# Optimization experiments

Measured on AMD Instinct MI355X. Metric: run time of the kernel, lower is better.

Reference implementation:

```python
import jax, jax.numpy as jnp
import numpy as np

N_NODES = 50000
N_EDGES = 800000
MUL = 16            # multiplicity of each irrep (16x0e + 16x1o)
RADIAL_IN = 8       # radial basis size
RADIAL_HID = 64
N_PATHS = 5         # TP paths: s*Y0->s, v.Yv->s, s*Yv->v, v*Y0->v, v x Yv->v
NUM_SPECIES = 4
AVG_NEIGH = 16.0


def setup_inputs() -> dict:
    key = jax.random.key(0)
    ks = jax.random.split(key, 16)
    inp = {
        'node_scalars': jax.random.normal(ks[0], (N_NODES, MUL), jnp.float32),
        'node_vectors': jax.random.normal(ks[1], (N_NODES, MUL * 3), jnp.float32),
        'edge_sh': jax.random.normal(ks[2], (N_EDGES, 4), jnp.float32),
        'radial_emb': jax.random.uniform(ks[3], (N_EDGES, RADIAL_IN), jnp.float32),
        'senders': jax.random.randint(ks[4], (N_EDGES,), 0, N_NODES, jnp.int32),
        'receivers': jax.random.randint(ks[5], (N_EDGES,), 0, N_NODES, jnp.int32),
        'species': jax.random.randint(ks[6], (N_NODES,), 0, NUM_SPECIES, jnp.int32),
        # learned params (fan-in scaled)
        'W_in_s': jax.random.normal(ks[7], (MUL, MUL), jnp.float32) / np.sqrt(MUL),
        'W_in_v': jax.random.normal(ks[8], (MUL, MUL), jnp.float32) / np.sqrt(MUL),
        'mlp_w1': jax.random.normal(ks[9], (RADIAL_IN, RADIAL_HID), jnp.float32) / np.sqrt(RADIAL_IN),
        'mlp_b1': jnp.zeros((RADIAL_HID,), jnp.float32),
        'mlp_w2': jax.random.normal(ks[10], (RADIAL_HID, N_PATHS * MUL), jnp.float32) / np.sqrt(RADIAL_HID),
        'W_out_s': jax.random.normal(ks[11], (2 * MUL, 2 * MUL), jnp.float32) / np.sqrt(2 * MUL),
        'W_out_v': jax.random.normal(ks[12], (3 * MUL, MUL), jnp.float32) / np.sqrt(3 * MUL),
        'sc_s': jax.random.normal(ks[13], (NUM_SPECIES, MUL, 2 * MUL), jnp.float32) / np.sqrt(MUL),
        'sc_v': jax.random.normal(ks[14], (NUM_SPECIES, MUL, MUL), jnp.float32) / np.sqrt(MUL),
    }
    return inp


def reference(node_scalars, node_vectors, edge_sh, radial_emb, senders, receivers,
              species, W_in_s, W_in_v, mlp_w1, mlp_b1, mlp_w2, W_out_s, W_out_v,
              sc_s, sc_v):
    N = node_scalars.shape[0]
    inv_sqrt_deg = 1.0 / np.sqrt(AVG_NEIGH)

    # ---- input per-irrep linear ----
    s = node_scalars @ W_in_s                                  # [N,16]
    v_in = node_vectors.reshape(N, MUL, 3)
    v = jnp.einsum('nuc,uw->nwc', v_in, W_in_v)                # [N,16,3]

    # ---- gather sender features ----
    xs = s[senders]                                            # [E,16]
    xv = v[senders]                                            # [E,16,3]
    Y0 = edge_sh[:, :1]                                        # [E,1] l=0 SH
    Yv = edge_sh[:, 1:4]                                       # [E,3] l=1 SH

    # ---- radial MLP -> per-path tensor-product weights ----
    h = jax.nn.silu(radial_emb @ mlp_w1 + mlp_b1)              # [E,64]
    w = (h @ mlp_w2).reshape(-1, N_PATHS, MUL)                 # [E,5,16]

    # ---- CG tensor product (uvu) messages ----
    m_s1 = w[:, 0] * xs * Y0                                   # 0e x 0e -> 0e
    m_s2 = w[:, 1] * jnp.einsum('euc,ec->eu', xv, Yv)          # 1o x 1o -> 0e (dot)
    m_v1 = w[:, 2, :, None] * xs[:, :, None] * Yv[:, None, :]  # 0e x 1o -> 1o
    m_v2 = w[:, 3, :, None] * xv * Y0[:, :, None]              # 1o x 0e -> 1o
    m_v3 = w[:, 4, :, None] * jnp.cross(xv, Yv[:, None, :])    # 1o x 1o -> 1o (cross)

    # ---- scatter-sum to receivers + neighbour normalization ----
    m_s = jnp.concatenate([m_s1, m_s2], axis=-1)               # [E,32]
    m_v = jnp.concatenate([m_v1, m_v2, m_v3], axis=1)          # [E,48,3]
    a_s = jax.ops.segment_sum(m_s, receivers, num_segments=N) * inv_sqrt_deg
    a_v = jax.ops.segment_sum(m_v, receivers, num_segments=N) * inv_sqrt_deg

    # ---- output per-irrep linear ----
    pre_s = a_s @ W_out_s                                      # [N,32]
    pre_v = jnp.einsum('nuc,uw->nwc', a_v, W_out_v)            # [N,16,3]

    # ---- species-dependent self connection ----
    pre_s = pre_s + jnp.einsum('nu,nuw->nw', node_scalars, sc_s[species])
    pre_v = pre_v + jnp.einsum('nuc,nuw->nwc', v_in, sc_v[species])

    # ---- gate nonlinearity ----
    out_s = jax.nn.silu(pre_s[:, :MUL])                        # scalar outputs
    gates = jax.nn.sigmoid(pre_s[:, MUL:])                     # gate scalars
    out_v = pre_v * gates[:, :, None]

    # ---- resnet ----
    out_s = out_s + node_scalars
    out_v = out_v + v_in

    return jnp.concatenate([out_s, out_v.reshape(N, MUL * 3)], axis=-1)
```

## Files before the change

kernel.cpp:

```cpp
#include <hip/hip_runtime.h>
#include <hip/hip_bf16.h>

typedef unsigned short u16;
typedef unsigned int   u32;
typedef _Float16 h2 __attribute__((ext_vector_type(2)));
typedef short s8v __attribute__((ext_vector_type(8)));
typedef float f4v __attribute__((ext_vector_type(4)));
typedef u16 u16x4 __attribute__((ext_vector_type(4)));

#define N_NODES 50000
#define N_EDGES 800000
#define NCH   2
#define RPC   25000
#define CHMAX 409600

#define RPB   250
#define NBINS 200
#define EPB   4096
#define NBB   ((N_EDGES+EPB-1)/EPB)

#define WB_W1H  0
#define WB_B1   256
#define WB_W2F  320
#define WB_WINS 2880
#define WB_WINV 3136
#define WB_WOS  3392
#define WB_WOV  4416
#define WB_SCS  5184
#define WB_SCV  7232
#define WB_FLAG 8256
#define OFF_SV16 8260
#define IDX_BCNT 1608260
#define IDX_BOF2 1608516
#define IDX_BCUR 1608772
#define IDX_OFFS 1658260
#define IDX_BUCK 1758262
#define IDX_EEID 2558264
#define OFF_ER16 3358264
#define OFF_WPA  3758264
#define OFF_WPB  16865464
#define OFF_YB   20142264
#define OFF_SND  21780664
#define ACC_OFF  21985464

__device__ __forceinline__ float bf2f(u16 v){
  union { u32 u; float f; } x; x.u = ((u32)v) << 16; return x.f;
}
__device__ __forceinline__ u16 f2bf(float f){
  u32 u = __float_as_uint(f);
  u32 lsb = (u >> 16) & 1u;
  u32 r = u + 0x7fffu + lsb;
  return (u16)(r >> 16);
}
__device__ __forceinline__ float ldx(const void* p, long long i, int isf){
  return isf ? ((const float*)p)[i] : bf2f(((const u16*)p)[i]);
}
__device__ __forceinline__ u32 pkh2(float a, float b){
  union { u32 u; h2 v; } x; x.v.x = (_Float16)a; x.v.y = (_Float16)b; return x.u;
}
__device__ __forceinline__ float dot2(h2 a, u32 w, float c){
  union { u32 u; h2 v; } x; x.u = w;
#if __has_builtin(__builtin_amdgcn_fdot2)
  return __builtin_amdgcn_fdot2(a, x.v, c, false);
#else
  return c + (float)a.x*(float)x.v.x + (float)a.y*(float)x.v.y;
#endif
}
__device__ __forceinline__ float sigmoidf_(float x){ return 1.f/(1.f + __expf(-x)); }

__global__ void detect_dtype(const u32* __restrict__ remb_raw, int* __restrict__ flag){
  int t = threadIdx.x;
  u32 w = remb_raw[t];
  u32 lo = w & 0xffffu, hi = w >> 16;
  int okl = ((lo & 0x8000u) == 0) && (((lo >> 7) & 0xffu) <= 126u);
  int okh = ((hi & 0x8000u) == 0) && (((hi >> 7) & 0xffu) <= 126u);
  unsigned long long bad = __ballot(!(okl && okh));
  if (t == 0) *flag = (bad != 0ull) ? 1 : 0;
}

__global__ void prep_weights(const void* __restrict__ w1, const void* __restrict__ b1g,
                             const void* __restrict__ w2, const void* __restrict__ wins,
                             const void* __restrict__ winv, const void* __restrict__ wos,
                             const void* __restrict__ wov, const void* __restrict__ scs,
                             const void* __restrict__ scv, float* __restrict__ wbuf,
                             const int* __restrict__ flag){
  int t = threadIdx.x;
  int isf = *flag;
  u32* w1h  = (u32*)(wbuf + WB_W1H);
  u16* w2f  = (u16*)(wbuf + WB_W2F);
  for (int idx=t; idx<256;  idx+=256){
    int j = idx>>2, ip = idx&3;
    w1h[idx] = pkh2(ldx(w1, (2*ip)*64+j, isf), ldx(w1, (2*ip+1)*64+j, isf));
  }
  for (int idx=t; idx<64;   idx+=256){ wbuf[WB_B1+idx]  = ldx(b1g, idx, isf); }
  for (int idx=t; idx<5120; idx+=256){
    int tt = idx >> 10;
    int rem = idx & 1023;
    int kh = rem >> 9;
    int rem2 = rem & 511;
    int ln = rem2 >> 3, j = rem2 & 7;
    int k = kh*32 + (ln>>4)*8 + j;
    int o = tt*16 + (ln&15);
    w2f[idx] = f2bf(ldx(w2, (long long)k*80 + o, isf));
  }
  for (int idx=t; idx<256;  idx+=256){ wbuf[WB_WINS+idx] = ldx(wins, idx, isf); }
  for (int idx=t; idx<256;  idx+=256){ wbuf[WB_WINV+idx] = ldx(winv, idx, isf); }
  for (int idx=t; idx<1024; idx+=256){ wbuf[WB_WOS+idx]  = ldx(wos, idx, isf); }
  for (int idx=t; idx<768;  idx+=256){ wbuf[WB_WOV+idx]  = ldx(wov, idx, isf); }
  for (int idx=t; idx<2048; idx+=256){ wbuf[WB_SCS+idx]  = ldx(scs, idx, isf); }
  for (int idx=t; idx<1024; idx+=256){ wbuf[WB_SCV+idx]  = ldx(scv, idx, isf); }
}

__global__ void __launch_bounds__(64) node_pre(
    const void* __restrict__ ns_g, const void* __restrict__ nv_g,
    const float* __restrict__ wbuf, u16* __restrict__ sv16,
    const int* __restrict__ flag){
  int n = blockIdx.x*64 + threadIdx.x;
  if (n >= N_NODES) return;
  int isf = *flag;
  float a[16], b[48];
  if (isf){
    const f4v* pa = (const f4v*)ns_g + (size_t)n*4;
    #pragma unroll
    for (int k=0;k<4;k++){
      f4v v = pa[k];
      a[k*4]=v[0]; a[k*4+1]=v[1]; a[k*4+2]=v[2]; a[k*4+3]=v[3];
    }
    const f4v* pb = (const f4v*)nv_g + (size_t)n*12;
    #pragma unroll
    for (int k=0;k<12;k++){
      f4v v = pb[k];
      b[k*4]=v[0]; b[k*4+1]=v[1]; b[k*4+2]=v[2]; b[k*4+3]=v[3];
    }
  } else {
    const s8v* pa = (const s8v*)ns_g + (size_t)n*2;
    #pragma unroll
    for (int k=0;k<2;k++){
      s8v v = pa[k];
      #pragma unroll
      for (int j=0;j<8;j++) a[k*8+j] = bf2f((u16)v[j]);
    }
    const s8v* pb = (const s8v*)nv_g + (size_t)n*6;
    #pragma unroll
    for (int k=0;k<6;k++){
      s8v v = pb[k];
      #pragma unroll
      for (int j=0;j<8;j++) b[k*8+j] = bf2f((u16)v[j]);
    }
  }
  const float* wins = wbuf + WB_WINS;
  const float* winv = wbuf + WB_WINV;
  float s[16];
  #pragma unroll
  for (int w=0;w<16;w++) s[w]=0.f;
  #pragma unroll
  for (int u=0;u<16;u++){
    float au = a[u];
    #pragma unroll
    for (int w=0;w<16;w++) s[w] += au * wins[u*16+w];
  }
  float v0[16], v1[16], v2[16];
  #pragma unroll
  for (int w=0;w<16;w++){ v0[w]=0.f; v1[w]=0.f; v2[w]=0.f; }
  #pragma unroll
  for (int u=0;u<16;u++){
    float bu0=b[u*3], bu1=b[u*3+1], bu2=b[u*3+2];
    #pragma unroll
    for (int w=0;w<16;w++){
      float wv = winv[u*16+w];
      v0[w] += bu0*wv; v1[w] += bu1*wv; v2[w] += bu2*wv;
    }
  }
  s8v* svp = (s8v*)(sv16 + (size_t)n*64);
  #pragma unroll
  for (int w=0;w<16;w+=2){
    s8v pk;
    pk[0]=(short)f2bf(s[w]);   pk[1]=(short)f2bf(v0[w]);
    pk[2]=(short)f2bf(v1[w]);  pk[3]=(short)f2bf(v2[w]);
    pk[4]=(short)f2bf(s[w+1]); pk[5]=(short)f2bf(v0[w+1]);
    pk[6]=(short)f2bf(v1[w+1]);pk[7]=(short)f2bf(v2[w+1]);
    svp[w>>1] = pk;
  }
}

__global__ void __launch_bounds__(256) bin_count(const int* __restrict__ receivers,
                                                 int* __restrict__ bcnt){
  __shared__ int lcnt[NBINS];
  int t = threadIdx.x;
  for (int i=t;i<NBINS;i+=256) lcnt[i]=0;
  __syncthreads();
  int base = blockIdx.x*EPB;
  for (int i=t;i<EPB;i+=256){
    int e = base+i;
    if (e<N_EDGES) atomicAdd(&lcnt[receivers[e]/RPB],1);
  }
  __syncthreads();
  for (int i=t;i<NBINS;i+=256) if (lcnt[i]) atomicAdd(&bcnt[i], lcnt[i]);
}

__global__ void bin_scan(const int* __restrict__ bcnt, int* __restrict__ binoff,
                         int* __restrict__ bincur, int* __restrict__ offs){
  __shared__ int lds[NBINS];
  int t=threadIdx.x;
  if (t<NBINS) lds[t]=bcnt[t];
  __syncthreads();
  for (int off=1; off<NBINS; off<<=1){
    int v = (t<NBINS && t>=off)? lds[t-off] : 0;
    __syncthreads();
    if (t<NBINS) lds[t]+=v;
    __syncthreads();
  }
  if (t<NBINS){ int ex = lds[t]-bcnt[t]; binoff[t]=ex; bincur[t]=ex; }
  if (t==0) offs[N_NODES] = N_EDGES;
}

__global__ void __launch_bounds__(256) bin_scatter(const int* __restrict__ receivers,
                 int* __restrict__ bincur, u32* __restrict__ eeid, u16* __restrict__ er){
  __shared__ int lcnt[NBINS], loff[NBINS], lcur[NBINS], gbase[NBINS];
  __shared__ u32 seid[EPB];
  __shared__ u16 sr[EPB];
  int t = threadIdx.x;
  for (int i=t;i<NBINS;i+=256) lcnt[i]=0;
  __syncthreads();
  int base = blockIdx.x*EPB;
  int r_[16];
  #pragma unroll
  for (int k=0;k<16;k++){
    int e = base + t + k*256;
    r_[k] = (e<N_EDGES)? receivers[e] : -1;
    if (r_[k]>=0) atomicAdd(&lcnt[r_[k]/RPB],1);
  }
  __syncthreads();
  if (t<NBINS) loff[t]=lcnt[t];
  __syncthreads();
  for (int off=1; off<NBINS; off<<=1){
    int v=(t<NBINS&&t>=off)?loff[t-off]:0;
    __syncthreads();
    if (t<NBINS) loff[t]+=v;
    __syncthreads();
  }
  if (t<NBINS){
    int ex=loff[t]-lcnt[t]; loff[t]=ex; lcur[t]=ex;
    gbase[t] = lcnt[t] ? atomicAdd(&bincur[t], lcnt[t]) : 0;
  }
  __syncthreads();
  #pragma unroll
  for (int k=0;k<16;k++){
    if (r_[k]>=0){
      int b=r_[k]/RPB;
      int p=atomicAdd(&lcur[b],1);
      seid[p]=(u32)(base + t + k*256);
      sr[p]=(u16)r_[k];
    }
  }
  __syncthreads();
  int rem = N_EDGES - base;
  int tot = rem < EPB ? rem : EPB;
  for (int i=t;i<tot;i+=256){
    int b = sr[i]/RPB;
    int dst = gbase[b] + (i - loff[b]);
    eeid[dst]=seid[i]; er[dst]=sr[i];
  }
}

__global__ void __launch_bounds__(256) bin_finalize(const u32* __restrict__ eeid,
        const u16* __restrict__ er, const int* __restrict__ binoff,
        const int* __restrict__ bcnt, int* __restrict__ offs, int* __restrict__ bucket){
  __shared__ int deg[RPB], pfx[RPB], lcur[RPB];
  int b=blockIdx.x, t=threadIdx.x;
  int beg=binoff[b], cnt=bcnt[b];
  for (int i=t;i<RPB;i+=256) deg[i]=0;
  __syncthreads();
  int r0=b*RPB;
  for (int i=t;i<cnt;i+=256) atomicAdd(&deg[er[beg+i]-r0],1);
  __syncthreads();
  if (t<RPB) pfx[t]=deg[t];
  __syncthreads();
  for (int off=1; off<RPB; off<<=1){
    int v=(t<RPB&&t>=off)?pfx[t-off]:0;
    __syncthreads();
    if (t<RPB) pfx[t]+=v;
    __syncthreads();
  }
  if (t<RPB){
    int ex=pfx[t]-deg[t]; pfx[t]=ex; lcur[t]=ex;
    offs[r0+t]=beg+ex;
  }
  __syncthreads();
  for (int i=t;i<cnt;i+=256){
    int rr = er[beg+i]-r0;
    int k = atomicAdd(&lcur[rr],1);
    bucket[beg+k] = (int)eeid[beg+i];
  }
}

__global__ void __launch_bounds__(256) pass1_w(
    const int* __restrict__ bucket, const int* __restrict__ offs,
    const void* __restrict__ remb, const void* __restrict__ edge_sh,
    const int* __restrict__ senders, const float* __restrict__ wbuf,
    u16* __restrict__ wpA, u16* __restrict__ wpB,
    float* __restrict__ ybf, u16* __restrict__ snd16,
    int rlo, const int* __restrict__ flag){
  __shared__ u16 hlds[4*16*72];
  int tid = threadIdx.x;
  int lane = tid & 63, wid = tid >> 6;
  int isf = *flag;
  int chunkBeg = offs[rlo], chunkEnd = offs[rlo + RPC];
  int r0e = chunkBeg + (blockIdx.x*4 + wid)*16;
  if (r0e >= chunkEnd) return;
  u16* hw = hlds + wid*(16*72);
  int e = lane & 15, q = lane >> 4;

  int er = r0e + e;
  int eid = (er < chunkEnd) ? bucket[er] : 0;
  if (q == 0 && er < chunkEnd){
    size_t widx = (size_t)(er - chunkBeg);
    snd16[widx] = (u16)senders[eid];
    f4v y;
    if (isf){
      y = ((const f4v*)edge_sh)[eid];
    } else {
      u16x4 yb = ((const u16x4*)edge_sh)[eid];
      y[0]=bf2f(yb[0]); y[1]=bf2f(yb[1]); y[2]=bf2f(yb[2]); y[3]=bf2f(yb[3]);
    }
    ((f4v*)ybf)[widx] = y;
  }
  float re[8];
  if (isf){
    f4v ra = ((const f4v*)remb)[(size_t)eid*2];
    f4v rb = ((const f4v*)remb)[(size_t)eid*2+1];
    re[0]=ra[0]; re[1]=ra[1]; re[2]=ra[2]; re[3]=ra[3];
    re[4]=rb[0]; re[5]=rb[1]; re[6]=rb[2]; re[7]=rb[3];
  } else {
    s8v r8 = ((const s8v*)remb)[eid];
    #pragma unroll
    for (int i=0;i<8;i++) re[i] = bf2f((u16)r8[i]);
  }
  h2 reh[4];
  #pragma unroll
  for (int ip=0;ip<4;ip++){ reh[ip].x=(_Float16)re[2*ip]; reh[ip].y=(_Float16)re[2*ip+1]; }
  const u32* w1h = (const u32*)(wbuf + WB_W1H);
  const float* b1 = wbuf + WB_B1;
  #pragma unroll
  for (int jj=0;jj<16;jj++){
    int j = q*16 + jj;
    float a = b1[j];
    #pragma unroll
    for (int ip=0;ip<4;ip++) a = dot2(reh[ip], w1h[j*4+ip], a);
    a = a * sigmoidf_(a);
    hw[e*72 + j] = f2bf(a);
  }
  asm volatile("s_waitcnt lgkmcnt(0)" ::: "memory");

  const u16* w2f = (const u16*)(wbuf + WB_W2F);
  s8v bfr[5][2];
  #pragma unroll
  for (int t=0;t<5;t++)
    #pragma unroll
    for (int kh=0;kh<2;kh++)
      bfr[t][kh] = *(const s8v*)(w2f + ((t*2+kh)*64 + lane)*8);

  f4v acc[5];
  #pragma unroll
  for (int t=0;t<5;t++) acc[t] = (f4v){0.f,0.f,0.f,0.f};
  #pragma unroll
  for (int kh=0;kh<2;kh++){
    s8v af = *(const s8v*)(hw + e*72 + kh*32 + q*8);
    #pragma unroll
    for (int t=0;t<5;t++)
      acc[t] = __builtin_amdgcn_mfma_f32_16x16x32_bf16(af, bfr[t][kh], acc[t], 0,0,0);
  }
  int n = lane & 15;
  #pragma unroll
  for (int r=0;r<4;r++){
    int er2 = r0e + q*4 + r;
    if (er2 < chunkEnd){
      size_t widx = (size_t)(er2 - chunkBeg);
      u16x4 pk4;
      pk4[0]=f2bf(acc[0][r]); pk4[1]=f2bf(acc[1][r]);
      pk4[2]=f2bf(acc[2][r]); pk4[3]=f2bf(acc[3][r]);
      ((u16x4*)wpA)[widx*16 + n] = pk4;
      wpB[widx*16 + n] = f2bf(acc[4][r]);
    }
  }
}

__global__ void __launch_bounds__(256, 4) pass2_reduce(
    const int* __restrict__ offs,
    const u16* __restrict__ sv16, const u16* __restrict__ wpA,
    const u16* __restrict__ wpB, const float* __restrict__ ybf,
    const u16* __restrict__ snd16, float* __restrict__ accbuf,
    int rlo){
  __shared__ float part[4][176];
  int tid = threadIdx.x;
  int lane = tid & 63, wid = tid >> 6;
  int u = lane & 15, q = lane >> 4;
  int pr = wid >> 1;
  int wsub = wid & 1;
  int r = rlo + blockIdx.x*2 + pr;
  int chunkBeg = offs[rlo];
  int beg = offs[r], end = offs[r+1];
  float As0=0.f,As1=0.f;
  float Av00=0.f,Av01=0.f,Av02=0.f, Av10=0.f,Av11=0.f,Av12=0.f, Av20=0.f,Av21=0.f,Av22=0.f;
  auto body = [&](int rank){
    size_t li = (size_t)(rank - chunkBeg);
    f4v y = ((const f4v*)ybf)[li];
    float Y0=y[0], Yv0=y[1], Yv1=y[2], Yv2=y[3];
    int snd = snd16[li];
    u16x4 wv = ((const u16x4*)wpA)[li*16 + u];
    float w0=bf2f(wv[0]), w1=bf2f(wv[1]), w2=bf2f(wv[2]), w3=bf2f(wv[3]);
    float w4=bf2f(wpB[li*16 + u]);
    u16x4 sv = *(const u16x4*)(sv16 + ((size_t)snd*16 + u)*4);
    float xs=bf2f(sv[0]), x0=bf2f(sv[1]), x1=bf2f(sv[2]), x2=bf2f(sv[3]);
    As0 += w0*xs*Y0;
    As1 += w1*(x0*Yv0 + x1*Yv1 + x2*Yv2);
    float t1 = w2*xs;  Av00 += t1*Yv0; Av01 += t1*Yv1; Av02 += t1*Yv2;
    float t2 = w3*Y0;  Av10 += t2*x0;  Av11 += t2*x1;  Av12 += t2*x2;
    Av20 += w4*(x1*Yv2 - x2*Yv1);
    Av21 += w4*(x2*Yv0 - x0*Yv2);
    Av22 += w4*(x0*Yv1 - x1*Yv0);
  };
  int rank = beg + wsub*4 + q;
  for (; rank + 8 < end; rank += 16){ body(rank); body(rank+8); }
  if (rank < end) body(rank);
  #define RED2(x) { x += __shfl_xor(x,16); x += __shfl_xor(x,32); }
  RED2(As0) RED2(As1)
  RED2(Av00) RED2(Av01) RED2(Av02)
  RED2(Av10) RED2(Av11) RED2(Av12)
  RED2(Av20) RED2(Av21) RED2(Av22)
  #undef RED2
  if (q == 0){
    float* pp = part[wid];
    pp[u]=As0;      pp[16+u]=As1;
    pp[32+u]=Av00;  pp[48+u]=Av10;  pp[64+u]=Av20;
    pp[80+u]=Av01;  pp[96+u]=Av11;  pp[112+u]=Av21;
    pp[128+u]=Av02; pp[144+u]=Av12; pp[160+u]=Av22;
  }
  __syncthreads();
  for (int i = tid; i < 352; i += 256){
    int pr2 = i / 176, idx = i - pr2*176;
    int rr = blockIdx.x*2 + pr2;
    accbuf[(size_t)rr*176 + idx] = part[pr2*2][idx] + part[pr2*2+1][idx];
  }
}

__global__ void __launch_bounds__(256) pass2_epilogue(
    const float* __restrict__ accbuf, const float* __restrict__ wbuf,
    const void* __restrict__ ns_g, const void* __restrict__ nv_g,
    const int* __restrict__ species, void* __restrict__ out,
    int rlo, const int* __restrict__ flag){
  __shared__ float sb[16*176 + 16*16 + 16*48];
  int tid = threadIdx.x;
  int isf = *flag;
  int n0 = rlo + blockIdx.x*16;
  int rem = rlo + RPC - n0;
  int nblk = rem < 16 ? rem : 16;
  {
    int tot = nblk*176;
    const float* src = accbuf + (size_t)(n0 - rlo)*176;
    for (int i=tid; i<tot; i+=256) sb[i] = src[i];
    float* nsb = sb + 2816;
    for (int i=tid; i<nblk*16; i+=256)
      nsb[i] = ldx(ns_g, (long long)n0*16 + i, isf);
    float* vinb = sb + 2816 + 256;
    for (int i=tid; i<nblk*48; i+=256)
      vinb[i] = ldx(nv_g, (long long)n0*48 + i, isf);
  }
  __syncthreads();
  int g = tid >> 4, u = tid & 15;
  if (g >= nblk) return;
  int nn = n0 + g;
  const float* bin  = sb + g*176;
  const float* nsb  = sb + 2816 + g*16;
  const float* vinb = sb + 2816 + 256 + g*48;
  int sp = species[nn];
  const float* wos = wbuf + WB_WOS;
  const float* scs = wbuf + WB_SCS + sp*512;
  const float* wov = wbuf + WB_WOV;
  const float* scv = wbuf + WB_SCV + sp*256;
  float p0 = 0.f, p1 = 0.f;
  #pragma unroll
  for (int j=0;j<32;j++){
    float a = bin[j]*0.25f;
    p0 += a*wos[j*32+u];
    p1 += a*wos[j*32+16+u];
  }
  #pragma unroll
  for (int j=0;j<16;j++){
    float nu = nsb[j];
    p0 += nu*scs[j*32+u];
    p1 += nu*scs[j*32+16+u];
  }
  float gate = sigmoidf_(p1);
  float os = p0*sigmoidf_(p0) + nsb[u];
  float pv0, pv1, pv2;
  {
    float a0=0.f, a1=0.f, a2=0.f;
    #pragma unroll
    for (int j=0;j<48;j++){
      float wv = wov[j*16+u];
      a0 += bin[32 + 0*48 + j]*0.25f*wv;
      a1 += bin[32 + 1*48 + j]*0.25f*wv;
      a2 += bin[32 + 2*48 + j]*0.25f*wv;
    }
    #pragma unroll
    for (int j=0;j<16;j++){
      float sv = scv[j*16+u];
      a0 += vinb[j*3+0]*sv;
      a1 += vinb[j*3+1]*sv;
      a2 += vinb[j*3+2]*sv;
    }
    pv0 = a0*gate + vinb[u*3+0];
    pv1 = a1*gate + vinb[u*3+1];
    pv2 = a2*gate + vinb[u*3+2];
  }
  if (isf){
    float* orow = (float*)out + (size_t)nn*64;
    orow[u] = os;
    orow[16 + u*3 + 0] = pv0;
    orow[16 + u*3 + 1] = pv1;
    orow[16 + u*3 + 2] = pv2;
  } else {
    u16* orow = (u16*)out + (size_t)nn*64;
    orow[u] = f2bf(os);
    orow[16 + u*3 + 0] = f2bf(pv0);
    orow[16 + u*3 + 1] = f2bf(pv1);
    orow[16 + u*3 + 2] = f2bf(pv2);
  }
}

extern "C" void kernel_launch(void* const* d_in, const int* in_sizes, int n_in,
                              void* d_out, int out_size, void* d_ws, size_t ws_size,
                              hipStream_t stream){
  const void* node_scalars = d_in[0];
  const void* node_vectors = d_in[1];
  const void* edge_sh      = d_in[2];
  const void* radial_emb   = d_in[3];
  const int* senders      = (const int*)d_in[4];
  const int* receivers    = (const int*)d_in[5];
  const int* species      = (const int*)d_in[6];
  const void* W_in_s  = d_in[7];
  const void* W_in_v  = d_in[8];
  const void* mlp_w1  = d_in[9];
  const void* mlp_b1  = d_in[10];
  const void* mlp_w2  = d_in[11];
  const void* W_out_s = d_in[12];
  const void* W_out_v = d_in[13];
  const void* sc_s    = d_in[14];
  const void* sc_v    = d_in[15];

  float* wsf  = (float*)d_ws;
  int*   wsi  = (int*)d_ws;
  u32*   wsu  = (u32*)d_ws;
  float* wbuf = wsf;
  u16*   sv16 = (u16*)(wsu + OFF_SV16);
  int*   bcnt = wsi + IDX_BCNT;
  int*   bof2 = wsi + IDX_BOF2;
  int*   bcur = wsi + IDX_BCUR;
  int*   offs = wsi + IDX_OFFS;
  int*   buck = wsi + IDX_BUCK;
  u32*   eeid = wsu + IDX_EEID;
  u16*   er16 = (u16*)(wsu + OFF_ER16);
  u16*   wpA  = (u16*)(wsu + OFF_WPA);
  u16*   wpB  = (u16*)(wsu + OFF_WPB);
  float* ybf  = wsf + OFF_YB;
  u16*   snd16= (u16*)(wsu + OFF_SND);
  float* accb = wsf + ACC_OFF;
  int*   flag = (int*)(wbuf + WB_FLAG);

  detect_dtype<<<1,64,0,stream>>>((const u32*)radial_emb, flag);
  hipMemsetAsync(bcnt, 0, NBINS*sizeof(int), stream);
  prep_weights<<<1,256,0,stream>>>(mlp_w1, mlp_b1, mlp_w2, W_in_s, W_in_v,
                                   W_out_s, W_out_v, sc_s, sc_v, wbuf, flag);
  node_pre<<<(N_NODES+63)/64,64,0,stream>>>(node_scalars, node_vectors, wbuf,
                                            sv16, flag);
  bin_count<<<NBB,256,0,stream>>>(receivers, bcnt);
  bin_scan<<<1,256,0,stream>>>(bcnt, bof2, bcur, offs);
  bin_scatter<<<NBB,256,0,stream>>>(receivers, bcur, eeid, er16);
  bin_finalize<<<NBINS,256,0,stream>>>(eeid, er16, bof2, bcnt, offs, buck);
  for (int c = 0; c < NCH; c++){
    int rlo = c * RPC;
    pass1_w<<<CHMAX/64, 256, 0, stream>>>(buck, offs, radial_emb, edge_sh, senders,
                                          wbuf, wpA, wpB, ybf, snd16, rlo, flag);
    pass2_reduce<<<RPC/2, 256, 0, stream>>>(offs, sv16, wpA, wpB, ybf, snd16,
                                            accb, rlo);
    pass2_epilogue<<<(RPC+15)/16, 256, 0, stream>>>(accb, wbuf, node_scalars,
                                                    node_vectors, species,
                                                    d_out, rlo, flag);
  }
}
```

Baseline: 376.2 us.

## Pack per-edge inputs into contiguous records and fuse epilogue into reduce

Adds a pack_edges kernel that copies radial embedding, spherical harmonics and sender into one 64-byte (fp32) or 32-byte (bf16) record per edge. pass1_w then does one contiguous gather per sorted edge instead of three scattered ones. The node epilogue (output linear, self-connection, gate, residual) moves into pass2_reduce, which drops the accbuf round trip and one launch per chunk. The cost is an extra full pass over the edge inputs, and only 32 threads per block run the epilogue, which may leave the tail of pass2_reduce poorly occupied.

```diff
diff --git a/kernel.cpp b/kernel.cpp
--- a/kernel.cpp
+++ b/kernel.cpp
@@ -41,7 +41,7 @@
 #define OFF_WPB  16865464
 #define OFF_YB   20142264
 #define OFF_SND  21780664
-#define ACC_OFF  21985464
+#define OFF_REC  21985472
 
 __device__ __forceinline__ float bf2f(u16 v){
   union { u32 u; float f; } x; x.u = ((u32)v) << 16; return x.f;
@@ -183,6 +183,31 @@
   }
 }
 
+__global__ void __launch_bounds__(256) pack_edges(
+    const void* __restrict__ remb, const void* __restrict__ edge_sh,
+    const int* __restrict__ senders, u32* __restrict__ rec,
+    const int* __restrict__ flag){
+  int e = blockIdx.x*256 + threadIdx.x;
+  if (e >= N_EDGES) return;
+  int isf = *flag;
+  if (isf){
+    u32* r = rec + (size_t)e*16;
+    f4v ra = ((const f4v*)remb)[(size_t)e*2];
+    f4v rb = ((const f4v*)remb)[(size_t)e*2+1];
+    ((f4v*)r)[0] = ra;
+    ((f4v*)r)[1] = rb;
+    ((f4v*)r)[2] = ((const f4v*)edge_sh)[e];
+    r[12] = (u32)senders[e];
+  } else {
+    u32* r = rec + (size_t)e*8;
+    *(s8v*)r = ((const s8v*)remb)[e];
+    const u32* ys = (const u32*)edge_sh + (size_t)e*2;
+    r[4]=ys[0]; r[5]=ys[1];
+    r[6] = (u32)senders[e];
+    r[7] = 0;
+  }
+}
+
 __global__ void __launch_bounds__(256) bin_count(const int* __restrict__ receivers,
                                                  int* __restrict__ bcnt){
   __shared__ int lcnt[NBINS];
@@ -296,8 +321,7 @@
 
 __global__ void __launch_bounds__(256) pass1_w(
     const int* __restrict__ bucket, const int* __restrict__ offs,
-    const void* __restrict__ remb, const void* __restrict__ edge_sh,
-    const int* __restrict__ senders, const float* __restrict__ wbuf,
+    const u32* __restrict__ rec, const float* __restrict__ wbuf,
     u16* __restrict__ wpA, u16* __restrict__ wpB,
     float* __restrict__ ybf, u16* __restrict__ snd16,
     int rlo, const int* __restrict__ flag){
@@ -313,28 +337,32 @@
 
   int er = r0e + e;
   int eid = (er < chunkEnd) ? bucket[er] : 0;
-  if (q == 0 && er < chunkEnd){
-    size_t widx = (size_t)(er - chunkBeg);
-    snd16[widx] = (u16)senders[eid];
-    f4v y;
-    if (isf){
-      y = ((const f4v*)edge_sh)[eid];
-    } else {
-      u16x4 yb = ((const u16x4*)edge_sh)[eid];
-      y[0]=bf2f(yb[0]); y[1]=bf2f(yb[1]); y[2]=bf2f(yb[2]); y[3]=bf2f(yb[3]);
-    }
-    ((f4v*)ybf)[widx] = y;
-  }
   float re[8];
   if (isf){
-    f4v ra = ((const f4v*)remb)[(size_t)eid*2];
-    f4v rb = ((const f4v*)remb)[(size_t)eid*2+1];
+    const u32* r = rec + (size_t)eid*16;
+    f4v ra = ((const f4v*)r)[0];
+    f4v rb = ((const f4v*)r)[1];
     re[0]=ra[0]; re[1]=ra[1]; re[2]=ra[2]; re[3]=ra[3];
     re[4]=rb[0]; re[5]=rb[1]; re[6]=rb[2]; re[7]=rb[3];
+    if (q == 0 && er < chunkEnd){
+      size_t widx = (size_t)(er - chunkBeg);
+      ((f4v*)ybf)[widx] = ((const f4v*)r)[2];
+      snd16[widx] = (u16)r[12];
+    }
   } else {
-    s8v r8 = ((const s8v*)remb)[eid];
+    const u32* r = rec + (size_t)eid*8;
+    s8v r8 = *(const s8v*)r;
     #pragma unroll
     for (int i=0;i<8;i++) re[i] = bf2f((u16)r8[i]);
+    if (q == 0 && er < chunkEnd){
+      size_t widx = (size_t)(er - chunkBeg);
+      u32 y0 = r[4], y1 = r[5];
+      f4v y;
+      y[0]=bf2f((u16)(y0 & 0xffffu)); y[1]=bf2f((u16)(y0 >> 16));
+      y[2]=bf2f((u16)(y1 & 0xffffu)); y[3]=bf2f((u16)(y1 >> 16));
+      ((f4v*)ybf)[widx] = y;
+      snd16[widx] = (u16)r[6];
+    }
   }
   h2 reh[4];
   #pragma unroll
@@ -389,17 +417,28 @@
     const int* __restrict__ offs,
     const u16* __restrict__ sv16, const u16* __restrict__ wpA,
     const u16* __restrict__ wpB, const float* __restrict__ ybf,
-    const u16* __restrict__ snd16, float* __restrict__ accbuf,
-    int rlo){
+    const u16* __restrict__ snd16, const float* __restrict__ wbuf,
+    const void* __restrict__ ns_g, const void* __restrict__ nv_g,
+    const int* __restrict__ species, void* __restrict__ out,
+    int rlo, const int* __restrict__ flag){
   __shared__ float part[4][176];
+  __shared__ float nsb[2][16], vinb[2][48];
+  __shared__ int spl[2];
   int tid = threadIdx.x;
   int lane = tid & 63, wid = tid >> 6;
   int u = lane & 15, q = lane >> 4;
   int pr = wid >> 1;
   int wsub = wid & 1;
-  int r = rlo + blockIdx.x*2 + pr;
+  int isf = *flag;
+  int r0n = rlo + blockIdx.x*2;
+  int r = r0n + pr;
   int chunkBeg = offs[rlo];
   int beg = offs[r], end = offs[r+1];
+  for (int i=tid; i<32; i+=256)
+    nsb[i>>4][i&15] = ldx(ns_g, (long long)(r0n + (i>>4))*16 + (i&15), isf);
+  for (int i=tid; i<96; i+=256)
+    vinb[i/48][i%48] = ldx(nv_g, (long long)(r0n + i/48)*48 + (i%48), isf);
+  if (tid < 2) spl[tid] = species[r0n + tid];
   float As0=0.f,As1=0.f;
   float Av00=0.f,Av01=0.f,Av02=0.f, Av10=0.f,Av11=0.f,Av12=0.f, Av20=0.f,Av21=0.f,Av22=0.f;
   auto body = [&](int rank){
@@ -437,95 +476,65 @@
     pp[128+u]=Av02; pp[144+u]=Av12; pp[160+u]=Av22;
   }
   __syncthreads();
-  for (int i = tid; i < 352; i += 256){
-    int pr2 = i / 176, idx = i - pr2*176;
-    int rr = blockIdx.x*2 + pr2;
-    accbuf[(size_t)rr*176 + idx] = part[pr2*2][idx] + part[pr2*2+1][idx];
-  }
-}
-
-__global__ void __launch_bounds__(256) pass2_epilogue(
-    const float* __restrict__ accbuf, const float* __restrict__ wbuf,
-    const void* __restrict__ ns_g, const void* __restrict__ nv_g,
-    const int* __restrict__ species, void* __restrict__ out,
-    int rlo, const int* __restrict__ flag){
-  __shared__ float sb[16*176 + 16*16 + 16*48];
-  int tid = threadIdx.x;
-  int isf = *flag;
-  int n0 = rlo + blockIdx.x*16;
-  int rem = rlo + RPC - n0;
-  int nblk = rem < 16 ? rem : 16;
-  {
-    int tot = nblk*176;
-    const float* src = accbuf + (size_t)(n0 - rlo)*176;
-    for (int i=tid; i<tot; i+=256) sb[i] = src[i];
-    float* nsb = sb + 2816;
-    for (int i=tid; i<nblk*16; i+=256)
-      nsb[i] = ldx(ns_g, (long long)n0*16 + i, isf);
-    float* vinb = sb + 2816 + 256;
-    for (int i=tid; i<nblk*48; i+=256)
-      vinb[i] = ldx(nv_g, (long long)n0*48 + i, isf);
-  }
-  __syncthreads();
-  int g = tid >> 4, u = tid & 15;
-  if (g >= nblk) return;
-  int nn = n0 + g;
-  const float* bin  = sb + g*176;
-  const float* nsb  = sb + 2816 + g*16;
-  const float* vinb = sb + 2816 + 256 + g*48;
-  int sp = species[nn];
-  const float* wos = wbuf + WB_WOS;
-  const float* scs = wbuf + WB_SCS + sp*512;
-  const float* wov = wbuf + WB_WOV;
-  const float* scv = wbuf + WB_SCV + sp*256;
-  float p0 = 0.f, p1 = 0.f;
-  #pragma unroll
-  for (int j=0;j<32;j++){
-    float a = bin[j]*0.25f;
-    p0 += a*wos[j*32+u];
-    p1 += a*wos[j*32+16+u];
-  }
-  #pragma unroll
-  for (int j=0;j<16;j++){
-    float nu = nsb[j];
-    p0 += nu*scs[j*32+u];
-    p1 += nu*scs[j*32+16+u];
-  }
-  float gate = sigmoidf_(p1);
-  float os = p0*sigmoidf_(p0) + nsb[u];
-  float pv0, pv1, pv2;
-  {
+
+  if (tid < 32){
+    int pr2 = tid >> 4, u2 = tid & 15;
+    int nn = r0n + pr2;
+    const float* pa = part[pr2*2];
+    const float* pb = part[pr2*2+1];
+    int sp = spl[pr2];
+    const float* wos = wbuf + WB_WOS;
+    const float* scs = wbuf + WB_SCS + sp*512;
+    const float* wov = wbuf + WB_WOV;
+    const float* scv = wbuf + WB_SCV + sp*256;
+    const float* nsp = nsb[pr2];
+    const float* vip = vinb[pr2];
+    float p0 = 0.f, p1 = 0.f;
+    #pragma unroll
+    for (int j=0;j<32;j++){
+      float a = (pa[j]+pb[j])*0.25f;
+      p0 += a*wos[j*32+u2];
+      p1 += a*wos[j*32+16+u2];
+    }
+    #pragma unroll
+    for (int j=0;j<16;j++){
+      float nu = nsp[j];
+      p0 += nu*scs[j*32+u2];
+      p1 += nu*scs[j*32+16+u2];
+    }
+    float gate = sigmoidf_(p1);
+    float os = p0*sigmoidf_(p0) + nsp[u2];
     float a0=0.f, a1=0.f, a2=0.f;
     #pragma unroll
     for (int j=0;j<48;j++){
-      float wv = wov[j*16+u];
-      a0 += bin[32 + 0*48 + j]*0.25f*wv;
-      a1 += bin[32 + 1*48 + j]*0.25f*wv;
-      a2 += bin[32 + 2*48 + j]*0.25f*wv;
+      float wv = wov[j*16+u2];
+      a0 += (pa[32 + 0*48 + j]+pb[32 + 0*48 + j])*0.25f*wv;
+      a1 += (pa[32 + 1*48 + j]+pb[32 + 1*48 + j])*0.25f*wv;
+      a2 += (pa[32 + 2*48 + j]+pb[32 + 2*48 + j])*0.25f*wv;
     }
     #pragma unroll
     for (int j=0;j<16;j++){
-      float sv = scv[j*16+u];
-      a0 += vinb[j*3+0]*sv;
-      a1 += vinb[j*3+1]*sv;
-      a2 += vinb[j*3+2]*sv;
-    }
-    pv0 = a0*gate + vinb[u*3+0];
-    pv1 = a1*gate + vinb[u*3+1];
-    pv2 = a2*gate + vinb[u*3+2];
-  }
-  if (isf){
-    float* orow = (float*)out + (size_t)nn*64;
-    orow[u] = os;
-    orow[16 + u*3 + 0] = pv0;
-    orow[16 + u*3 + 1] = pv1;
-    orow[16 + u*3 + 2] = pv2;
-  } else {
-    u16* orow = (u16*)out + (size_t)nn*64;
-    orow[u] = f2bf(os);
-    orow[16 + u*3 + 0] = f2bf(pv0);
-    orow[16 + u*3 + 1] = f2bf(pv1);
-    orow[16 + u*3 + 2] = f2bf(pv2);
+      float sv = scv[j*16+u2];
+      a0 += vip[j*3+0]*sv;
+      a1 += vip[j*3+1]*sv;
+      a2 += vip[j*3+2]*sv;
+    }
+    float pv0 = a0*gate + vip[u2*3+0];
+    float pv1 = a1*gate + vip[u2*3+1];
+    float pv2 = a2*gate + vip[u2*3+2];
+    if (isf){
+      float* orow = (float*)out + (size_t)nn*64;
+      orow[u2] = os;
+      orow[16 + u2*3 + 0] = pv0;
+      orow[16 + u2*3 + 1] = pv1;
+      orow[16 + u2*3 + 2] = pv2;
+    } else {
+      u16* orow = (u16*)out + (size_t)nn*64;
+      orow[u2] = f2bf(os);
+      orow[16 + u2*3 + 0] = f2bf(pv0);
+      orow[16 + u2*3 + 1] = f2bf(pv1);
+      orow[16 + u2*3 + 2] = f2bf(pv2);
+    }
   }
 }
 
@@ -565,7 +574,7 @@
   u16*   wpB  = (u16*)(wsu + OFF_WPB);
   float* ybf  = wsf + OFF_YB;
   u16*   snd16= (u16*)(wsu + OFF_SND);
-  float* accb = wsf + ACC_OFF;
+  u32*   rec  = wsu + OFF_REC;
   int*   flag = (int*)(wbuf + WB_FLAG);
 
   detect_dtype<<<1,64,0,stream>>>((const u32*)radial_emb, flag);
@@ -574,18 +583,18 @@
                                    W_out_s, W_out_v, sc_s, sc_v, wbuf, flag);
   node_pre<<<(N_NODES+63)/64,64,0,stream>>>(node_scalars, node_vectors, wbuf,
                                             sv16, flag);
+  pack_edges<<<(N_EDGES+255)/256,256,0,stream>>>(radial_emb, edge_sh, senders,
+                                                 rec, flag);
   bin_count<<<NBB,256,0,stream>>>(receivers, bcnt);
   bin_scan<<<1,256,0,stream>>>(bcnt, bof2, bcur, offs);
   bin_scatter<<<NBB,256,0,stream>>>(receivers, bcur, eeid, er16);
   bin_finalize<<<NBINS,256,0,stream>>>(eeid, er16, bof2, bcnt, offs, buck);
   for (int c = 0; c < NCH; c++){
     int rlo = c * RPC;
-    pass1_w<<<CHMAX/64, 256, 0, stream>>>(buck, offs, radial_emb, edge_sh, senders,
-                                          wbuf, wpA, wpB, ybf, snd16, rlo, flag);
+    pass1_w<<<CHMAX/64, 256, 0, stream>>>(buck, offs, rec, wbuf,
+                                          wpA, wpB, ybf, snd16, rlo, flag);
     pass2_reduce<<<RPC/2, 256, 0, stream>>>(offs, sv16, wpA, wpB, ybf, snd16,
-                                            accb, rlo);
-    pass2_epilogue<<<(RPC+15)/16, 256, 0, stream>>>(accb, wbuf, node_scalars,
-                                                    node_vectors, species,
-                                                    d_out, rlo, flag);
-  }
-}
+                                            wbuf, node_scalars, node_vectors,
+                                            species, d_out, rlo, flag);
+  }
+}
```

Result: slower. 502.8 us (+33.7%).
